# Optimization experiments

Hardware: AMD Instinct MI355X
Metric: run time of the kernel (lower is better)

## Reference

```python
import jax, jax.numpy as jnp
import numpy as np

N_NODES = 50000
N_EDGES = 800000
N_GRAPHS = 512
IN_CH, HID_CH, OUT_CH, N_CLASSES = 128, 64, 64, 10


def gcn_conv(x, src, dst, ew, W, b, n_nodes):
    """PyG GCNConv: add self-loops (weight 1), symmetric normalization, x @ W, scatter-add at dst, + bias."""
    xw = x @ W  # [N, out]
    loop = jnp.arange(n_nodes, dtype=src.dtype)
    src_f = jnp.concatenate([src, loop])
    dst_f = jnp.concatenate([dst, loop])
    ew_f = jnp.concatenate([ew, jnp.ones((n_nodes,), dtype=ew.dtype)])
    deg = jax.ops.segment_sum(ew_f, dst_f, num_segments=n_nodes)  # [N]
    dinv = jnp.where(deg > 0, jax.lax.rsqrt(deg), 0.0)
    norm = dinv[src_f] * ew_f * dinv[dst_f]  # [E+N]
    msg = norm[:, None] * xw[src_f]  # gather + scale
    out = jax.ops.segment_sum(msg, dst_f, num_segments=n_nodes)  # scatter-add
    return out + b


def setup_inputs() -> dict:
    key = jax.random.key(0)
    ks = jax.random.split(key, 12)
    x = jax.random.normal(ks[0], (N_NODES, IN_CH), dtype=jnp.float32)
    edge_index = jax.random.randint(ks[1], (2, N_EDGES), 0, N_NODES, dtype=jnp.int64)
    edge_attr = jax.random.uniform(ks[2], (N_EDGES,), dtype=jnp.float32)
    batch = jnp.sort(jax.random.randint(ks[3], (N_NODES,), 0, N_GRAPHS, dtype=jnp.int64))
    def glorot(k, shape):
        lim = np.sqrt(6.0 / (shape[0] + shape[1]))
        return jax.random.uniform(k, shape, jnp.float32, -lim, lim)
    W1 = glorot(ks[4], (IN_CH, HID_CH))
    b1 = jnp.zeros((HID_CH,), jnp.float32)
    W2 = glorot(ks[5], (HID_CH, OUT_CH))
    b2 = jnp.zeros((OUT_CH,), jnp.float32)
    LW1 = glorot(ks[6], (OUT_CH, 32))
    Lb1 = jnp.zeros((32,), jnp.float32)
    LW2 = glorot(ks[7], (32, N_CLASSES))
    Lb2 = jnp.zeros((N_CLASSES,), jnp.float32)
    return {"x": x, "edge_index": edge_index, "edge_attr": edge_attr, "batch": batch,
            "W1": W1, "b1": b1, "W2": W2, "b2": b2,
            "LW1": LW1, "Lb1": Lb1, "LW2": LW2, "Lb2": Lb2}


def reference(x, edge_index, edge_attr, batch, W1, b1, W2, b2, LW1, Lb1, LW2, Lb2):
    src, dst = edge_index[0], edge_index[1]
    h = gcn_conv(x, src, dst, edge_attr, W1, b1, N_NODES)
    h = jax.nn.relu(h)
    h = gcn_conv(h, src, dst, edge_attr, W2, b2, N_NODES)
    # global mean pool over graphs
    sums = jax.ops.segment_sum(h, batch, num_segments=N_GRAPHS)  # [G, OUT]
    cnt = jax.ops.segment_sum(jnp.ones((N_NODES,), h.dtype), batch, num_segments=N_GRAPHS)
    pooled = sums / jnp.maximum(cnt, 1.0)[:, None]
    # head (dropout treated as identity for deterministic reference)
    h1 = pooled @ LW1 + Lb1
    return h1 @ LW2 + Lb2
```

## Files before the change

### kernel.cpp

```cpp
#include <hip/hip_runtime.h>
#include <hip/hip_bf16.h>

static constexpr int NN = 50000;
static constexpr int NE = 800000;
static constexpr int NG = 512;
static constexpr int NB = 196;
static constexpr int HIST_BLOCKS = (NE + 255) / 256;
static constexpr int GEMM_BLOCKS = (NN + 63) / 64;

__device__ __forceinline__ float bfu(ushort u) {
    return __uint_as_float((unsigned)u << 16);
}
__device__ __forceinline__ ushort fbf(float f) {
    return __hip_bfloat16_raw(__float2bfloat16(f)).x;
}


__global__ void zero_kernel(float* __restrict__ p, int n) {
    int i = blockIdx.x * blockDim.x + threadIdx.x;
    if (i < n) p[i] = 0.f;
}

template <int K, bool BF16IN>
__device__ __forceinline__ void gemm_body(const void* __restrict__ Xv,
                                          const float* __restrict__ W,
                                          ushort* __restrict__ out,
                                          int row0, float Xs[][68], float* Ws) {
    for (int i = threadIdx.x; i < K * 16; i += 256)
        ((float4*)Ws)[i] = ((const float4*)W)[i];
    int tx = threadIdx.x & 15, ty = threadIdx.x >> 4;
    float acc[4][4] = {};
    for (int kb = 0; kb < K; kb += 64) {
        __syncthreads();
        if constexpr (BF16IN) {
            const ushort* X = (const ushort*)Xv;
            for (int i = threadIdx.x; i < 512; i += 256) {
                int r = i >> 3, g = i & 7;
                int gr = row0 + r; if (gr >= NN) gr = NN - 1;
                uint4 v = *(const uint4*)(X + (long long)gr * K + kb + g * 8);
                float4 f0, f1;
                f0.x = __uint_as_float(v.x << 16); f0.y = __uint_as_float(v.x & 0xffff0000u);
                f0.z = __uint_as_float(v.y << 16); f0.w = __uint_as_float(v.y & 0xffff0000u);
                f1.x = __uint_as_float(v.z << 16); f1.y = __uint_as_float(v.z & 0xffff0000u);
                f1.z = __uint_as_float(v.w << 16); f1.w = __uint_as_float(v.w & 0xffff0000u);
                *(float4*)&Xs[r][g * 8] = f0;
                *(float4*)&Xs[r][g * 8 + 4] = f1;
            }
        } else {
            const float* X = (const float*)Xv;
            for (int i = threadIdx.x; i < 1024; i += 256) {
                int r = i >> 4, k4 = i & 15;
                int gr = row0 + r; if (gr >= NN) gr = NN - 1;
                float4 v = *(const float4*)(X + (long long)gr * K + kb + k4 * 4);
                *(float4*)&Xs[r][k4 * 4] = v;
            }
        }
        __syncthreads();
#pragma unroll 16
        for (int k = 0; k < 64; ++k) {
            float4 wv = *(const float4*)&Ws[(kb + k) * 64 + tx * 4];
            float x0 = Xs[ty * 4 + 0][k];
            float x1 = Xs[ty * 4 + 1][k];
            float x2 = Xs[ty * 4 + 2][k];
            float x3 = Xs[ty * 4 + 3][k];
            acc[0][0] = fmaf(x0, wv.x, acc[0][0]); acc[0][1] = fmaf(x0, wv.y, acc[0][1]);
            acc[0][2] = fmaf(x0, wv.z, acc[0][2]); acc[0][3] = fmaf(x0, wv.w, acc[0][3]);
            acc[1][0] = fmaf(x1, wv.x, acc[1][0]); acc[1][1] = fmaf(x1, wv.y, acc[1][1]);
            acc[1][2] = fmaf(x1, wv.z, acc[1][2]); acc[1][3] = fmaf(x1, wv.w, acc[1][3]);
            acc[2][0] = fmaf(x2, wv.x, acc[2][0]); acc[2][1] = fmaf(x2, wv.y, acc[2][1]);
            acc[2][2] = fmaf(x2, wv.z, acc[2][2]); acc[2][3] = fmaf(x2, wv.w, acc[2][3]);
            acc[3][0] = fmaf(x3, wv.x, acc[3][0]); acc[3][1] = fmaf(x3, wv.y, acc[3][1]);
            acc[3][2] = fmaf(x3, wv.z, acc[3][2]); acc[3][3] = fmaf(x3, wv.w, acc[3][3]);
        }
    }
#pragma unroll
    for (int j = 0; j < 4; ++j) {
        int r = row0 + ty * 4 + j;
        if (r < NN) {
            ushort4 sv;
            sv.x = fbf(acc[j][0]); sv.y = fbf(acc[j][1]);
            sv.z = fbf(acc[j][2]); sv.w = fbf(acc[j][3]);
            *(ushort4*)(out + (long long)r * 64 + tx * 4) = sv;
        }
    }
}

__global__ __launch_bounds__(256) void hist_gemm_kernel(const int* __restrict__ dst,
                                                        const float* __restrict__ ew,
                                                        unsigned long long* __restrict__ h,
                                                        int* __restrict__ rank,
                                                        const float* __restrict__ X,
                                                        const float* __restrict__ W,
                                                        ushort* __restrict__ out) {
    __shared__ float Xs[64][68];
    __shared__ float Ws[128 * 64];
    if (blockIdx.x < HIST_BLOCKS) {
        int e = blockIdx.x * 256 + threadIdx.x;
        if (e >= NE) return;
        int d = dst[e];
        unsigned int fx = __float2uint_rn(ew[e] * 1048576.0f);
        unsigned long long pack = (1ULL << 40) | (unsigned long long)fx;
        unsigned long long old = atomicAdd(&h[d], pack);
        rank[e] = (int)(old >> 40);
        return;
    }
    gemm_body<128, false>(X, W, out, (blockIdx.x - HIST_BLOCKS) * 64, Xs, Ws);
}

template <int K, bool BF16IN>
__global__ __launch_bounds__(256) void gemm_kernel(const void* __restrict__ Xv,
                                                   const float* __restrict__ W,
                                                   ushort* __restrict__ out) {
    __shared__ float Xs[64][68];
    __shared__ float Ws[K * 64];
    gemm_body<K, BF16IN>(Xv, W, out, blockIdx.x * 64, Xs, Ws);
}

__global__ __launch_bounds__(256) void dinv_scanA_kernel(const unsigned long long* __restrict__ h,
                                                         float* __restrict__ dinv,
                                                         int* __restrict__ partial) {
    int i = blockIdx.x * 256 + threadIdx.x;
    int cnt = 0;
    if (i < NN) {
        unsigned long long v = h[i];
        cnt = (int)(v >> 40);
        float deg = (float)(v & ((1ULL << 40) - 1)) * (1.0f / 1048576.0f) + 1.0f;
        dinv[i] = 1.0f / sqrtf(deg);
    }
    __shared__ int wsum[4];
    int lane = threadIdx.x & 63, wid = threadIdx.x >> 6;
    int v = cnt;
#pragma unroll
    for (int off = 32; off > 0; off >>= 1) v += __shfl_down(v, (unsigned)off, 64);
    if (lane == 0) wsum[wid] = v;
    __syncthreads();
    if (threadIdx.x == 0) partial[blockIdx.x] = wsum[0] + wsum[1] + wsum[2] + wsum[3];
}

__device__ __forceinline__ int block_scan_inclusive(int v, int* wtot) {
    int lane = threadIdx.x & 63, wid = threadIdx.x >> 6;
    int inc = v;
#pragma unroll
    for (int off = 1; off < 64; off <<= 1) {
        int n = __shfl_up(inc, (unsigned)off, 64);
        if (lane >= off) inc += n;
    }
    if (lane == 63) wtot[wid] = inc;
    __syncthreads();
    int add = 0;
    for (int w = 0; w < wid; ++w) add += wtot[w];
    return inc + add;
}

__global__ __launch_bounds__(256) void scanC_bounds_kernel(const unsigned long long* __restrict__ h,
                                                           const int* __restrict__ partial,
                                                           int* __restrict__ rowptr,
                                                           const int* __restrict__ batch,
                                                           int* __restrict__ gbeg,
                                                           int* __restrict__ gend) {
    __shared__ int wtot[4];
    __shared__ int poff_s;
    int t = threadIdx.x;
    if (t < 64) {
        int s = 0;
        for (int i = t; i < (int)blockIdx.x; i += 64) s += partial[i];
#pragma unroll
        for (int off = 32; off > 0; off >>= 1) s += __shfl_down(s, (unsigned)off, 64);
        if (t == 0) poff_s = s;
    }
    int i = blockIdx.x * 256 + t;
    int v = (i < NN) ? (int)(h[i] >> 40) : 0;
    int incl = block_scan_inclusive(v, wtot);
    if (i < NN) {
        rowptr[i + 1] = poff_s + incl;
        int g = batch[i];
        if (i == 0 || batch[i - 1] != g) gbeg[g] = i;
        if (i == NN - 1 || batch[i + 1] != g) gend[g] = i + 1;
    }
    if (i == 0) rowptr[0] = 0;
}

__global__ __launch_bounds__(256) void scatter_kernel(const int* __restrict__ src,
                                                      const int* __restrict__ dst,
                                                      const float* __restrict__ ew,
                                                      const float* __restrict__ dinv,
                                                      const int* __restrict__ rowptr,
                                                      const int* __restrict__ rank,
                                                      int2* __restrict__ epack) {
    int e = blockIdx.x * blockDim.x + threadIdx.x;
    if (e >= NE) return;
    int s = src[e], d = dst[e];
    int pos = rowptr[d] + rank[e];
    float coef = dinv[s] * ew[e];
    epack[pos] = make_int2(s, __float_as_int(coef));
}

template <bool RELU>
__global__ __launch_bounds__(256) void agg_kernel(const ushort* __restrict__ xw,
                                                  const int* __restrict__ rowptr,
                                                  const int2* __restrict__ epack,
                                                  const float* __restrict__ dinv,
                                                  const float* __restrict__ bias,
                                                  ushort* __restrict__ out) {
    int node = blockIdx.x * 4 + (threadIdx.x >> 6);
    if (node >= NN) return;
    int lane = threadIdx.x & 63;
    int q = lane >> 4;
    int l = lane & 15;
    int beg = rowptr[node], end = rowptr[node + 1];
    float a0 = 0.f, a1 = 0.f, a2 = 0.f, a3 = 0.f;
    float b0 = 0.f, b1 = 0.f, b2 = 0.f, b3 = 0.f;
    int j = beg + q;
    for (; j + 4 < end; j += 8) {
        int2 pA = epack[j];
        int2 pB = epack[j + 4];
        ushort4 uA = *(const ushort4*)(xw + pA.x * 64 + 4 * l);
        ushort4 uB = *(const ushort4*)(xw + pB.x * 64 + 4 * l);
        float wA = __int_as_float(pA.y);
        float wB = __int_as_float(pB.y);
        a0 = fmaf(wA, bfu(uA.x), a0); a1 = fmaf(wA, bfu(uA.y), a1);
        a2 = fmaf(wA, bfu(uA.z), a2); a3 = fmaf(wA, bfu(uA.w), a3);
        b0 = fmaf(wB, bfu(uB.x), b0); b1 = fmaf(wB, bfu(uB.y), b1);
        b2 = fmaf(wB, bfu(uB.z), b2); b3 = fmaf(wB, bfu(uB.w), b3);
    }
    if (j < end) {
        int2 pA = epack[j];
        ushort4 uA = *(const ushort4*)(xw + pA.x * 64 + 4 * l);
        float wA = __int_as_float(pA.y);
        a0 = fmaf(wA, bfu(uA.x), a0); a1 = fmaf(wA, bfu(uA.y), a1);
        a2 = fmaf(wA, bfu(uA.z), a2); a3 = fmaf(wA, bfu(uA.w), a3);
    }
    a0 += b0; a1 += b1; a2 += b2; a3 += b3;
    a0 += __shfl_xor(a0, 16); a0 += __shfl_xor(a0, 32);
    a1 += __shfl_xor(a1, 16); a1 += __shfl_xor(a1, 32);
    a2 += __shfl_xor(a2, 16); a2 += __shfl_xor(a2, 32);
    a3 += __shfl_xor(a3, 16); a3 += __shfl_xor(a3, 32);
    if (q == 0) {
        float di = dinv[node];
        float d2 = di * di;
        ushort4 us = *(const ushort4*)(xw + node * 64 + 4 * l);
        float4 bv = *(const float4*)(bias + 4 * l);
        float o0 = fmaf(di, a0, fmaf(d2, bfu(us.x), bv.x));
        float o1 = fmaf(di, a1, fmaf(d2, bfu(us.y), bv.y));
        float o2 = fmaf(di, a2, fmaf(d2, bfu(us.z), bv.z));
        float o3 = fmaf(di, a3, fmaf(d2, bfu(us.w), bv.w));
        if (RELU) {
            o0 = fmaxf(o0, 0.f); o1 = fmaxf(o1, 0.f);
            o2 = fmaxf(o2, 0.f); o3 = fmaxf(o3, 0.f);
        }
        ushort4 sv;
        sv.x = fbf(o0); sv.y = fbf(o1); sv.z = fbf(o2); sv.w = fbf(o3);
        *(ushort4*)(out + node * 64 + 4 * l) = sv;
    }
}

__global__ __launch_bounds__(256) void poolhead_kernel(const ushort* __restrict__ h,
                                                       const int* __restrict__ gbeg,
                                                       const int* __restrict__ gend,
                                                       const float* __restrict__ LW1,
                                                       const float* __restrict__ Lb1,
                                                       const float* __restrict__ LW2,
                                                       const float* __restrict__ Lb2,
                                                       float* __restrict__ out) {
    __shared__ float pp[4][64];
    __shared__ float p[64];
    __shared__ float t1[32];
    int g = blockIdx.x, t = threadIdx.x;
    int lane = t & 63, wid = t >> 6;
    int b = gbeg[g], e = gend[g];
    float acc = 0.f;
    for (int i = b + wid; i < e; i += 4) acc += bfu(h[i * 64 + lane]);
    pp[wid][lane] = acc;
    __syncthreads();
    if (t < 64) {
        float s = pp[0][t] + pp[1][t] + pp[2][t] + pp[3][t];
        p[t] = s / fmaxf((float)(e - b), 1.0f);
    }
    __syncthreads();
    if (t < 32) {
        float a = Lb1[t];
#pragma unroll
        for (int k = 0; k < 64; ++k) a = fmaf(p[k], LW1[k * 32 + t], a);
        t1[t] = a;
    }
    __syncthreads();
    if (t < 10) {
        float a = Lb2[t];
#pragma unroll
        for (int j = 0; j < 32; ++j) a = fmaf(t1[j], LW2[j * 10 + t], a);
        out[g * 10 + t] = a;
    }
}


extern "C" void kernel_launch(void* const* d_in, const int* in_sizes, int n_in,
                              void* d_out, int out_size, void* d_ws, size_t ws_size,
                              hipStream_t stream) {
    const float* x     = (const float*)d_in[0];
    const int*   ei    = (const int*)d_in[1];
    const float* ew    = (const float*)d_in[2];
    const int*   batch = (const int*)d_in[3];
    const float* W1    = (const float*)d_in[4];
    const float* b1    = (const float*)d_in[5];
    const float* W2    = (const float*)d_in[6];
    const float* b2    = (const float*)d_in[7];
    const float* LW1   = (const float*)d_in[8];
    const float* Lb1   = (const float*)d_in[9];
    const float* LW2   = (const float*)d_in[10];
    const float* Lb2   = (const float*)d_in[11];

    const int* src = ei;
    const int* dst = ei + NE;

    float* ws = (float*)d_ws;
    unsigned long long* h64 = (unsigned long long*)ws;
    int*   gbeg   = (int*)(ws + 100096);
    int*   gend   = (int*)(ws + 100608);
    float* dinv   = ws + 101120;
    int*   rowptr = (int*)(ws + 151168);
    int*   partial= (int*)(ws + 201216);
    int2*  epack  = (int2*)(ws + 201472);
    ushort* xwA   = (ushort*)(ws + 1801472);
    ushort* h12   = (ushort*)(ws + 3401472);
    int*   rank   = (int*)(ws + 5001472);

    zero_kernel<<<(101120 + 255) / 256, 256, 0, stream>>>(ws, 101120);

    hist_gemm_kernel<<<HIST_BLOCKS + GEMM_BLOCKS, 256, 0, stream>>>(dst, ew, h64, rank,
                                                                    x, W1, xwA);
    dinv_scanA_kernel<<<NB, 256, 0, stream>>>(h64, dinv, partial);
    scanC_bounds_kernel<<<NB, 256, 0, stream>>>(h64, partial, rowptr, batch, gbeg, gend);
    scatter_kernel<<<(NE + 255) / 256, 256, 0, stream>>>(src, dst, ew, dinv, rowptr, rank, epack);

    agg_kernel<true><<<(NN + 3) / 4, 256, 0, stream>>>(xwA, rowptr, epack, dinv, b1, h12);

    gemm_kernel<64, true><<<GEMM_BLOCKS, 256, 0, stream>>>(h12, W2, xwA);
    agg_kernel<false><<<(NN + 3) / 4, 256, 0, stream>>>(xwA, rowptr, epack, dinv, b2, h12);

    poolhead_kernel<<<NG, 256, 0, stream>>>(h12, gbeg, gend, LW1, Lb1, LW2, Lb2, (float*)d_out);
}
```

Measured before the change: 244.5 us.

## Fuse histogram, GEMM1, scan and CSR scatter into one persistent kernel with grid barriers

Replaces four separate launches (hist+gemm, dinv/scanA, scanC, scatter) with one persistent 1024-block kernel that partitions blocks between GEMM tiles and edge histogram work. Stages are separated by a software grid barrier built on atomics. Edge ranks stay in registers instead of round-tripping through global memory, and W1 is staged in shared memory as bf16 to shrink LDS. The software barrier assumes all 1024 blocks are co-resident, which a plain launch does not guarantee and which could deadlock. The bf16 W1 also adds rounding error.

Result: slower. 651.9 us (+166.6%).

```diff
diff --git a/kernel.cpp b/kernel.cpp
--- a/kernel.cpp
+++ b/kernel.cpp
@@ -5,8 +5,13 @@
 static constexpr int NE = 800000;
 static constexpr int NG = 512;
 static constexpr int NB = 196;
-static constexpr int HIST_BLOCKS = (NE + 255) / 256;
-static constexpr int GEMM_BLOCKS = (NN + 63) / 64;
+
+static constexpr int GRID = 1024;
+static constexpr int GB = 391;
+static constexpr int HB = GRID - GB;
+static constexpr int HTHREADS = HB * 256;
+static constexpr int KPT = 5;
+static constexpr int NTILES = (NN + 63) / 64;
 
 __device__ __forceinline__ float bfu(ushort u) {
     return __uint_as_float((unsigned)u << 16);
@@ -15,62 +20,59 @@
     return __hip_bfloat16_raw(__float2bfloat16(f)).x;
 }
 
+__device__ __forceinline__ void gsync(int* bar, int target) {
+    __syncthreads();
+    if (threadIdx.x == 0) {
+        __threadfence();
+        atomicAdd(bar, 1);
+        while (__hip_atomic_load(bar, __ATOMIC_RELAXED, __HIP_MEMORY_SCOPE_AGENT) < target) {}
+        __threadfence();
+    }
+    __syncthreads();
+}
 
 __global__ void zero_kernel(float* __restrict__ p, int n) {
     int i = blockIdx.x * blockDim.x + threadIdx.x;
     if (i < n) p[i] = 0.f;
 }
 
-template <int K, bool BF16IN>
-__device__ __forceinline__ void gemm_body(const void* __restrict__ Xv,
-                                          const float* __restrict__ W,
-                                          ushort* __restrict__ out,
-                                          int row0, float Xs[][68], float* Ws) {
-    for (int i = threadIdx.x; i < K * 16; i += 256)
-        ((float4*)Ws)[i] = ((const float4*)W)[i];
+__device__ __forceinline__ void gemm128_body(const float* __restrict__ X,
+                                             ushort* __restrict__ out,
+                                             int row0, float (*Xs)[68],
+                                             const ushort* __restrict__ Wsb) {
     int tx = threadIdx.x & 15, ty = threadIdx.x >> 4;
     float acc[4][4] = {};
-    for (int kb = 0; kb < K; kb += 64) {
+    for (int kb = 0; kb < 128; kb += 64) {
         __syncthreads();
-        if constexpr (BF16IN) {
-            const ushort* X = (const ushort*)Xv;
-            for (int i = threadIdx.x; i < 512; i += 256) {
-                int r = i >> 3, g = i & 7;
-                int gr = row0 + r; if (gr >= NN) gr = NN - 1;
-                uint4 v = *(const uint4*)(X + (long long)gr * K + kb + g * 8);
-                float4 f0, f1;
-                f0.x = __uint_as_float(v.x << 16); f0.y = __uint_as_float(v.x & 0xffff0000u);
-                f0.z = __uint_as_float(v.y << 16); f0.w = __uint_as_float(v.y & 0xffff0000u);
-                f1.x = __uint_as_float(v.z << 16); f1.y = __uint_as_float(v.z & 0xffff0000u);
-                f1.z = __uint_as_float(v.w << 16); f1.w = __uint_as_float(v.w & 0xffff0000u);
-                *(float4*)&Xs[r][g * 8] = f0;
-                *(float4*)&Xs[r][g * 8 + 4] = f1;
+        for (int i = threadIdx.x; i < 1024; i += 256) {
+            int r = i >> 4, k4 = i & 15;
+            int gr = row0 + r; if (gr >= NN) gr = NN - 1;
+            *(float4*)&Xs[r][k4 * 4] = *(const float4*)(X + (long long)gr * 128 + kb + k4 * 4);
+        }
+        __syncthreads();
+#pragma unroll
+        for (int k4 = 0; k4 < 16; ++k4) {
+            float4 x0 = *(const float4*)&Xs[ty * 4 + 0][k4 * 4];
+            float4 x1 = *(const float4*)&Xs[ty * 4 + 1][k4 * 4];
+            float4 x2 = *(const float4*)&Xs[ty * 4 + 2][k4 * 4];
+            float4 x3 = *(const float4*)&Xs[ty * 4 + 3][k4 * 4];
+#pragma unroll
+            for (int kk = 0; kk < 4; ++kk) {
+                uint2 wu = *(const uint2*)&Wsb[(kb + k4 * 4 + kk) * 64 + tx * 4];
+                float w0 = __uint_as_float(wu.x << 16);
+                float w1 = __uint_as_float(wu.x & 0xffff0000u);
+                float w2 = __uint_as_float(wu.y << 16);
+                float w3 = __uint_as_float(wu.y & 0xffff0000u);
+                float xa = (&x0.x)[kk], xb = (&x1.x)[kk], xc = (&x2.x)[kk], xd = (&x3.x)[kk];
+                acc[0][0] = fmaf(xa, w0, acc[0][0]); acc[0][1] = fmaf(xa, w1, acc[0][1]);
+                acc[0][2] = fmaf(xa, w2, acc[0][2]); acc[0][3] = fmaf(xa, w3, acc[0][3]);
+                acc[1][0] = fmaf(xb, w0, acc[1][0]); acc[1][1] = fmaf(xb, w1, acc[1][1]);
+                acc[1][2] = fmaf(xb, w2, acc[1][2]); acc[1][3] = fmaf(xb, w3, acc[1][3]);
+                acc[2][0] = fmaf(xc, w0, acc[2][0]); acc[2][1] = fmaf(xc, w1, acc[2][1]);
+                acc[2][2] = fmaf(xc, w2, acc[2][2]); acc[2][3] = fmaf(xc, w3, acc[2][3]);
+                acc[3][0] = fmaf(xd, w0, acc[3][0]); acc[3][1] = fmaf(xd, w1, acc[3][1]);
+                acc[3][2] = fmaf(xd, w2, acc[3][2]); acc[3][3] = fmaf(xd, w3, acc[3][3]);
             }
-        } else {
-            const float* X = (const float*)Xv;
-            for (int i = threadIdx.x; i < 1024; i += 256) {
-                int r = i >> 4, k4 = i & 15;
-                int gr = row0 + r; if (gr >= NN) gr = NN - 1;
-                float4 v = *(const float4*)(X + (long long)gr * K + kb + k4 * 4);
-                *(float4*)&Xs[r][k4 * 4] = v;
-            }
-        }
-        __syncthreads();
-#pragma unroll 16
-        for (int k = 0; k < 64; ++k) {
-            float4 wv = *(const float4*)&Ws[(kb + k) * 64 + tx * 4];
-            float x0 = Xs[ty * 4 + 0][k];
-            float x1 = Xs[ty * 4 + 1][k];
-            float x2 = Xs[ty * 4 + 2][k];
-            float x3 = Xs[ty * 4 + 3][k];
-            acc[0][0] = fmaf(x0, wv.x, acc[0][0]); acc[0][1] = fmaf(x0, wv.y, acc[0][1]);
-            acc[0][2] = fmaf(x0, wv.z, acc[0][2]); acc[0][3] = fmaf(x0, wv.w, acc[0][3]);
-            acc[1][0] = fmaf(x1, wv.x, acc[1][0]); acc[1][1] = fmaf(x1, wv.y, acc[1][1]);
-            acc[1][2] = fmaf(x1, wv.z, acc[1][2]); acc[1][3] = fmaf(x1, wv.w, acc[1][3]);
-            acc[2][0] = fmaf(x2, wv.x, acc[2][0]); acc[2][1] = fmaf(x2, wv.y, acc[2][1]);
-            acc[2][2] = fmaf(x2, wv.z, acc[2][2]); acc[2][3] = fmaf(x2, wv.w, acc[2][3]);
-            acc[3][0] = fmaf(x3, wv.x, acc[3][0]); acc[3][1] = fmaf(x3, wv.y, acc[3][1]);
-            acc[3][2] = fmaf(x3, wv.z, acc[3][2]); acc[3][3] = fmaf(x3, wv.w, acc[3][3]);
         }
     }
 #pragma unroll
@@ -85,58 +87,6 @@
     }
 }
 
-__global__ __launch_bounds__(256) void hist_gemm_kernel(const int* __restrict__ dst,
-                                                        const float* __restrict__ ew,
-                                                        unsigned long long* __restrict__ h,
-                                                        int* __restrict__ rank,
-                                                        const float* __restrict__ X,
-                                                        const float* __restrict__ W,
-                                                        ushort* __restrict__ out) {
-    __shared__ float Xs[64][68];
-    __shared__ float Ws[128 * 64];
-    if (blockIdx.x < HIST_BLOCKS) {
-        int e = blockIdx.x * 256 + threadIdx.x;
-        if (e >= NE) return;
-        int d = dst[e];
-        unsigned int fx = __float2uint_rn(ew[e] * 1048576.0f);
-        unsigned long long pack = (1ULL << 40) | (unsigned long long)fx;
-        unsigned long long old = atomicAdd(&h[d], pack);
-        rank[e] = (int)(old >> 40);
-        return;
-    }
-    gemm_body<128, false>(X, W, out, (blockIdx.x - HIST_BLOCKS) * 64, Xs, Ws);
-}
-
-template <int K, bool BF16IN>
-__global__ __launch_bounds__(256) void gemm_kernel(const void* __restrict__ Xv,
-                                                   const float* __restrict__ W,
-                                                   ushort* __restrict__ out) {
-    __shared__ float Xs[64][68];
-    __shared__ float Ws[K * 64];
-    gemm_body<K, BF16IN>(Xv, W, out, blockIdx.x * 64, Xs, Ws);
-}
-
-__global__ __launch_bounds__(256) void dinv_scanA_kernel(const unsigned long long* __restrict__ h,
-                                                         float* __restrict__ dinv,
-                                                         int* __restrict__ partial) {
-    int i = blockIdx.x * 256 + threadIdx.x;
-    int cnt = 0;
-    if (i < NN) {
-        unsigned long long v = h[i];
-        cnt = (int)(v >> 40);
-        float deg = (float)(v & ((1ULL << 40) - 1)) * (1.0f / 1048576.0f) + 1.0f;
-        dinv[i] = 1.0f / sqrtf(deg);
-    }
-    __shared__ int wsum[4];
-    int lane = threadIdx.x & 63, wid = threadIdx.x >> 6;
-    int v = cnt;
-#pragma unroll
-    for (int off = 32; off > 0; off >>= 1) v += __shfl_down(v, (unsigned)off, 64);
-    if (lane == 0) wsum[wid] = v;
-    __syncthreads();
-    if (threadIdx.x == 0) partial[blockIdx.x] = wsum[0] + wsum[1] + wsum[2] + wsum[3];
-}
-
 __device__ __forceinline__ int block_scan_inclusive(int v, int* wtot) {
     int lane = threadIdx.x & 63, wid = threadIdx.x >> 6;
     int inc = v;
@@ -152,47 +102,152 @@
     return inc + add;
 }
 
-__global__ __launch_bounds__(256) void scanC_bounds_kernel(const unsigned long long* __restrict__ h,
-                                                           const int* __restrict__ partial,
-                                                           int* __restrict__ rowptr,
-                                                           const int* __restrict__ batch,
-                                                           int* __restrict__ gbeg,
-                                                           int* __restrict__ gend) {
+__global__ __launch_bounds__(256, 4) void coop_kernel(
+    const int* __restrict__ src, const int* __restrict__ dst,
+    const float* __restrict__ ew, const int* __restrict__ batch,
+    const float* __restrict__ X, const float* __restrict__ W1,
+    unsigned long long* __restrict__ h, float* __restrict__ dinv,
+    int* __restrict__ rowptr, int* __restrict__ partial,
+    int* __restrict__ gbeg, int* __restrict__ gend,
+    int2* __restrict__ epack, ushort* __restrict__ xw1, int* __restrict__ bar) {
+    __shared__ float Xs[64][68];
+    __shared__ ushort Wsb[128 * 64];
     __shared__ int wtot[4];
     __shared__ int poff_s;
-    int t = threadIdx.x;
-    if (t < 64) {
-        int s = 0;
-        for (int i = t; i < (int)blockIdx.x; i += 64) s += partial[i];
-#pragma unroll
-        for (int off = 32; off > 0; off >>= 1) s += __shfl_down(s, (unsigned)off, 64);
-        if (t == 0) poff_s = s;
-    }
-    int i = blockIdx.x * 256 + t;
-    int v = (i < NN) ? (int)(h[i] >> 40) : 0;
-    int incl = block_scan_inclusive(v, wtot);
-    if (i < NN) {
-        rowptr[i + 1] = poff_s + incl;
-        int g = batch[i];
-        if (i == 0 || batch[i - 1] != g) gbeg[g] = i;
-        if (i == NN - 1 || batch[i + 1] != g) gend[g] = i + 1;
-    }
-    if (i == 0) rowptr[0] = 0;
-}
-
-__global__ __launch_bounds__(256) void scatter_kernel(const int* __restrict__ src,
-                                                      const int* __restrict__ dst,
-                                                      const float* __restrict__ ew,
-                                                      const float* __restrict__ dinv,
-                                                      const int* __restrict__ rowptr,
-                                                      const int* __restrict__ rank,
-                                                      int2* __restrict__ epack) {
-    int e = blockIdx.x * blockDim.x + threadIdx.x;
-    if (e >= NE) return;
-    int s = src[e], d = dst[e];
-    int pos = rowptr[d] + rank[e];
-    float coef = dinv[s] * ew[e];
-    epack[pos] = make_int2(s, __float_as_int(coef));
+    int bid = blockIdx.x, t = threadIdx.x;
+    int rank[KPT];
+
+    if (bid < GB) {
+        for (int i = t; i < 128 * 16; i += 256) {
+            float4 w = ((const float4*)W1)[i];
+            ushort4 s; s.x = fbf(w.x); s.y = fbf(w.y); s.z = fbf(w.z); s.w = fbf(w.w);
+            *(ushort4*)&Wsb[i * 4] = s;
+        }
+        for (int tile = bid; tile < NTILES; tile += GB)
+            gemm128_body(X, xw1, tile * 64, Xs, Wsb);
+    } else {
+        int ht = (bid - GB) * 256 + t;
+#pragma unroll
+        for (int k = 0; k < KPT; ++k) {
+            int e = ht + k * HTHREADS;
+            if (e < NE) {
+                int d = dst[e];
+                unsigned int fx = __float2uint_rn(ew[e] * 1048576.0f);
+                unsigned long long old = atomicAdd(&h[d], (1ULL << 40) | (unsigned long long)fx);
+                rank[k] = (int)(old >> 40);
+            }
+        }
+    }
+    gsync(bar, GRID);
+
+    if (bid < NB) {
+        int i = bid * 256 + t;
+        int cnt = 0;
+        if (i < NN) {
+            unsigned long long v = h[i];
+            cnt = (int)(v >> 40);
+            float deg = (float)(v & ((1ULL << 40) - 1)) * (1.0f / 1048576.0f) + 1.0f;
+            dinv[i] = 1.0f / sqrtf(deg);
+        }
+        int lane = t & 63, wid = t >> 6;
+        int v = cnt;
+#pragma unroll
+        for (int off = 32; off > 0; off >>= 1) v += __shfl_down(v, (unsigned)off, 64);
+        if (lane == 0) wtot[wid] = v;
+        __syncthreads();
+        if (t == 0) partial[bid] = wtot[0] + wtot[1] + wtot[2] + wtot[3];
+    }
+    gsync(bar, 2 * GRID);
+
+    if (bid < NB) {
+        if (t < 64) {
+            int s = 0;
+            for (int i2 = t; i2 < bid; i2 += 64) s += partial[i2];
+#pragma unroll
+            for (int off = 32; off > 0; off >>= 1) s += __shfl_down(s, (unsigned)off, 64);
+            if (t == 0) poff_s = s;
+        }
+        int i = bid * 256 + t;
+        int v = (i < NN) ? (int)(h[i] >> 40) : 0;
+        int incl = block_scan_inclusive(v, wtot);
+        if (i < NN) {
+            rowptr[i + 1] = poff_s + incl;
+            int g = batch[i];
+            if (i == 0 || batch[i - 1] != g) gbeg[g] = i;
+            if (i == NN - 1 || batch[i + 1] != g) gend[g] = i + 1;
+        }
+        if (i == 0) rowptr[0] = 0;
+    }
+    gsync(bar, 3 * GRID);
+
+    if (bid >= GB) {
+        int ht = (bid - GB) * 256 + t;
+#pragma unroll
+        for (int k = 0; k < KPT; ++k) {
+            int e = ht + k * HTHREADS;
+            if (e < NE) {
+                int s = src[e], d = dst[e];
+                int pos = rowptr[d] + rank[k];
+                epack[pos] = make_int2(s, __float_as_int(dinv[s] * ew[e]));
+            }
+        }
+    }
+}
+
+__global__ __launch_bounds__(256) void gemm64_kernel(const ushort* __restrict__ X,
+                                                     const float* __restrict__ W,
+                                                     ushort* __restrict__ out) {
+    __shared__ float Xs[64][68];
+    __shared__ float Ws[64 * 64];
+    for (int i = threadIdx.x; i < 64 * 16; i += 256)
+        ((float4*)Ws)[i] = ((const float4*)W)[i];
+    int tx = threadIdx.x & 15, ty = threadIdx.x >> 4;
+    int row0 = blockIdx.x * 64;
+    float acc[4][4] = {};
+    __syncthreads();
+    for (int i = threadIdx.x; i < 512; i += 256) {
+        int r = i >> 3, g = i & 7;
+        int gr = row0 + r; if (gr >= NN) gr = NN - 1;
+        uint4 v = *(const uint4*)(X + (long long)gr * 64 + g * 8);
+        float4 f0, f1;
+        f0.x = __uint_as_float(v.x << 16); f0.y = __uint_as_float(v.x & 0xffff0000u);
+        f0.z = __uint_as_float(v.y << 16); f0.w = __uint_as_float(v.y & 0xffff0000u);
+        f1.x = __uint_as_float(v.z << 16); f1.y = __uint_as_float(v.z & 0xffff0000u);
+        f1.z = __uint_as_float(v.w << 16); f1.w = __uint_as_float(v.w & 0xffff0000u);
+        *(float4*)&Xs[r][g * 8] = f0;
+        *(float4*)&Xs[r][g * 8 + 4] = f1;
+    }
+    __syncthreads();
+#pragma unroll
+    for (int k4 = 0; k4 < 16; ++k4) {
+        float4 x0 = *(const float4*)&Xs[ty * 4 + 0][k4 * 4];
+        float4 x1 = *(const float4*)&Xs[ty * 4 + 1][k4 * 4];
+        float4 x2 = *(const float4*)&Xs[ty * 4 + 2][k4 * 4];
+        float4 x3 = *(const float4*)&Xs[ty * 4 + 3][k4 * 4];
+#pragma unroll
+        for (int kk = 0; kk < 4; ++kk) {
+            float4 wv = *(const float4*)&Ws[(k4 * 4 + kk) * 64 + tx * 4];
+            float xa = (&x0.x)[kk], xb = (&x1.x)[kk], xc = (&x2.x)[kk], xd = (&x3.x)[kk];
+            acc[0][0] = fmaf(xa, wv.x, acc[0][0]); acc[0][1] = fmaf(xa, wv.y, acc[0][1]);
+            acc[0][2] = fmaf(xa, wv.z, acc[0][2]); acc[0][3] = fmaf(xa, wv.w, acc[0][3]);
+            acc[1][0] = fmaf(xb, wv.x, acc[1][0]); acc[1][1] = fmaf(xb, wv.y, acc[1][1]);
+            acc[1][2] = fmaf(xb, wv.z, acc[1][2]); acc[1][3] = fmaf(xb, wv.w, acc[1][3]);
+            acc[2][0] = fmaf(xc, wv.x, acc[2][0]); acc[2][1] = fmaf(xc, wv.y, acc[2][1]);
+            acc[2][2] = fmaf(xc, wv.z, acc[2][2]); acc[2][3] = fmaf(xc, wv.w, acc[2][3]);
+            acc[3][0] = fmaf(xd, wv.x, acc[3][0]); acc[3][1] = fmaf(xd, wv.y, acc[3][1]);
+            acc[3][2] = fmaf(xd, wv.z, acc[3][2]); acc[3][3] = fmaf(xd, wv.w, acc[3][3]);
+        }
+    }
+#pragma unroll
+    for (int j = 0; j < 4; ++j) {
+        int r = row0 + ty * 4 + j;
+        if (r < NN) {
+            ushort4 sv;
+            sv.x = fbf(acc[j][0]); sv.y = fbf(acc[j][1]);
+            sv.z = fbf(acc[j][2]); sv.w = fbf(acc[j][3]);
+            *(ushort4*)(out + (long long)r * 64 + tx * 4) = sv;
+        }
+    }
 }
 
 template <bool RELU>
@@ -316,25 +371,22 @@
     unsigned long long* h64 = (unsigned long long*)ws;
     int*   gbeg   = (int*)(ws + 100096);
     int*   gend   = (int*)(ws + 100608);
-    float* dinv   = ws + 101120;
-    int*   rowptr = (int*)(ws + 151168);
-    int*   partial= (int*)(ws + 201216);
-    int2*  epack  = (int2*)(ws + 201472);
-    ushort* xwA   = (ushort*)(ws + 1801472);
-    ushort* h12   = (ushort*)(ws + 3401472);
-    int*   rank   = (int*)(ws + 5001472);
-
-    zero_kernel<<<(101120 + 255) / 256, 256, 0, stream>>>(ws, 101120);
-
-    hist_gemm_kernel<<<HIST_BLOCKS + GEMM_BLOCKS, 256, 0, stream>>>(dst, ew, h64, rank,
-                                                                    x, W1, xwA);
-    dinv_scanA_kernel<<<NB, 256, 0, stream>>>(h64, dinv, partial);
-    scanC_bounds_kernel<<<NB, 256, 0, stream>>>(h64, partial, rowptr, batch, gbeg, gend);
-    scatter_kernel<<<(NE + 255) / 256, 256, 0, stream>>>(src, dst, ew, dinv, rowptr, rank, epack);
+    int*   bar    = (int*)(ws + 101120);
+    float* dinv   = ws + 101376;
+    int*   rowptr = (int*)(ws + 151424);
+    int*   partial= (int*)(ws + 201472);
+    int2*  epack  = (int2*)(ws + 202496);
+    ushort* xwA   = (ushort*)(ws + 1802496);
+    ushort* h12   = (ushort*)(ws + 3402496);
+
+    zero_kernel<<<(101376 + 255) / 256, 256, 0, stream>>>(ws, 101376);
+
+    coop_kernel<<<GRID, 256, 0, stream>>>(src, dst, ew, batch, x, W1, h64, dinv,
+                                          rowptr, partial, gbeg, gend, epack, xwA, bar);
 
     agg_kernel<true><<<(NN + 3) / 4, 256, 0, stream>>>(xwA, rowptr, epack, dinv, b1, h12);
 
-    gemm_kernel<64, true><<<GEMM_BLOCKS, 256, 0, stream>>>(h12, W2, xwA);
+    gemm64_kernel<<<NTILES, 256, 0, stream>>>(h12, W2, xwA);
     agg_kernel<false><<<(NN + 3) / 4, 256, 0, stream>>>(xwA, rowptr, epack, dinv, b2, h12);
 
     poolhead_kernel<<<NG, 256, 0, stream>>>(h12, gbeg, gend, LW1, Lb1, LW2, Lb2, (float*)d_out);
```
